# Optimization experiments

Hardware: AMD Instinct MI355X
Metric: run time of the kernel (lower is better)

Reference implementation:

```python
import jax, jax.numpy as jnp
import numpy as np

HSIG_SCALE = 0.16666667  # matches MyHSigmoid's * 0.16666667

def setup_inputs() -> dict:
    key = jax.random.key(0)
    k = jax.random.split(key, 5)
    B, C, H, W, MID = 32, 256, 56, 56, 64
    return {
        "x": jax.random.normal(k[0], (B, C, H, W), dtype=jnp.float32),
        "w1": jax.random.normal(k[1], (MID, C), dtype=jnp.float32) * 0.05,
        "b1": jax.random.normal(k[2], (MID,), dtype=jnp.float32) * 0.05,
        "w2": jax.random.normal(k[3], (C, MID), dtype=jnp.float32) * 0.05,
        "b2": jax.random.normal(k[4], (C,), dtype=jnp.float32) * 0.05,
        "inject": 0, "current_epoch": 0, "counter": 0, "inject_index": 0,
    }

def reference(x, w1, b1, w2, b2, inject, current_epoch, counter, inject_index):
    # global average pool over H,W -> [B, C]
    pooled = jnp.mean(x, axis=(2, 3))
    # 1x1 conv reduce (GEMV) + ReLU
    h = jax.nn.relu(jnp.einsum('bc,mc->bm', pooled, w1) + b1)
    # 1x1 conv expand + hard-sigmoid (relu6(y+3) * 0.16666667)
    y = jnp.einsum('bm,cm->bc', h, w2) + b2
    gate = jnp.clip(y + 3.0, 0.0, 6.0) * HSIG_SCALE
    # broadcast channel gate over spatial dims
    return x * gate[:, :, None, None]
```

## Files before the change

### kernel.cpp

```cpp
#include <hip/hip_runtime.h>
#include <stdint.h>

#define BATCH 32
#define CH    256
#define MID   64
#define HW    3136
#define HWV   784

typedef __attribute__((ext_vector_type(4))) float fvec4;

__global__ __launch_bounds__(256) void se_pool(const fvec4* __restrict__ x,
                                               float* __restrict__ pooled) {
    const int p = blockIdx.x;
    const fvec4* base = x + (size_t)p * HWV;
    const int t = threadIdx.x;

    float sum = 0.0f;
    for (int i = t; i < HWV; i += 256) {
        fvec4 v = base[i];
        sum += v.x + v.y + v.z + v.w;
    }
    #pragma unroll
    for (int off = 32; off > 0; off >>= 1) sum += __shfl_down(sum, off, 64);

    __shared__ float part[4];
    if ((t & 63) == 0) part[t >> 6] = sum;
    __syncthreads();
    if (t == 0) {
        pooled[p] = (part[0] + part[1] + part[2] + part[3]) * (1.0f / (float)HW);
    }
}

__global__ __launch_bounds__(256) void se_gate_scale(
    const fvec4* __restrict__ x,
    const float* __restrict__ pooled,
    const float* __restrict__ w1, const float* __restrict__ b1,
    const float* __restrict__ w2, const float* __restrict__ b2,
    fvec4* __restrict__ out) {
    const int p = blockIdx.x;
    const int b = p >> 8;
    const int c = p & 255;
    const int t = threadIdx.x;
    const int m = t & 63;
    const int q = t >> 6;

    __shared__ float ps[CH];
    __shared__ float hp[4][MID];
    __shared__ float hs[MID];
    __shared__ float gsh;

    ps[t] = pooled[b * CH + t];
    __syncthreads();

    {
        float acc = 0.0f;
        const fvec4* wrow = (const fvec4*)(w1 + m * CH + q * 64);
        const float* pq = ps + q * 64;
        #pragma unroll
        for (int i = 0; i < 16; ++i) {
            fvec4 wv = wrow[i];
            acc += pq[4 * i + 0] * wv.x + pq[4 * i + 1] * wv.y +
                   pq[4 * i + 2] * wv.z + pq[4 * i + 3] * wv.w;
        }
        hp[q][m] = acc;
    }
    __syncthreads();
    if (t < MID) {
        hs[t] = fmaxf(b1[t] + hp[0][t] + hp[1][t] + hp[2][t] + hp[3][t], 0.0f);
    }
    __syncthreads();
    if (t < 64) {
        float v = hs[t] * w2[c * MID + t];
        #pragma unroll
        for (int off = 32; off > 0; off >>= 1) v += __shfl_down(v, off, 64);
        if (t == 0) {
            gsh = fminf(fmaxf(v + b2[c] + 3.0f, 0.0f), 6.0f) * 0.16666667f;
        }
    }
    __syncthreads();
    const float g = gsh;

    const fvec4* xb = x + (size_t)p * HWV;
    fvec4* ob = out + (size_t)p * HWV;
    for (int i = t; i < HWV; i += 256) {
        fvec4 v = xb[i];
        fvec4 r = { v.x * g, v.y * g, v.z * g, v.w * g };
        __builtin_nontemporal_store(r, ob + i);
    }
}

extern "C" void kernel_launch(void* const* d_in, const int* in_sizes, int n_in,
                              void* d_out, int out_size, void* d_ws, size_t ws_size,
                              hipStream_t stream) {
    (void)in_sizes; (void)n_in; (void)out_size; (void)ws_size;

    const float* x  = (const float*)d_in[0];
    const float* w1 = (const float*)d_in[1];
    const float* b1 = (const float*)d_in[2];
    const float* w2 = (const float*)d_in[3];
    const float* b2 = (const float*)d_in[4];

    float* pooled = (float*)d_ws;

    se_pool<<<BATCH * CH, 256, 0, stream>>>((const fvec4*)x, pooled);
    se_gate_scale<<<BATCH * CH, 256, 0, stream>>>((const fvec4*)x, pooled,
                                                  w1, b1, w2, b2, (fvec4*)d_out);
}
```

Measured before the change: 247.0 us.

## Fold first GEMV into pooling via atomics and prefetch x before gate compute

The pooling kernel now multiplies each pooled channel value by its w1 column and atomically accumulates into a per-batch hidden pre-activation buffer (zeroed with a memset). The first GEMV is no longer recomputed in every one of the 8192 scale blocks. The scale kernel issues its loads of x into registers before the gate computation, so memory latency overlaps the small GEMV and sync, and its loop is fully unrolled. The cost is 64 atomics per block with contention on 2048 addresses, plus an extra memset launch, and float atomics make the summation order nondeterministic.

```diff
diff --git a/kernel.cpp b/kernel.cpp
--- a/kernel.cpp
+++ b/kernel.cpp
@@ -9,12 +9,15 @@
 
 typedef __attribute__((ext_vector_type(4))) float fvec4;
 
-__global__ __launch_bounds__(256) void se_pool(const fvec4* __restrict__ x,
-                                               float* __restrict__ pooled) {
+__global__ __launch_bounds__(256) void se_pool_h(const fvec4* __restrict__ x,
+                                                 const float* __restrict__ w1,
+                                                 float* __restrict__ hpre) {
     const int p = blockIdx.x;
-    const fvec4* base = x + (size_t)p * HWV;
+    const int b = p >> 8;
+    const int c = p & 255;
     const int t = threadIdx.x;
 
+    const fvec4* base = x + (size_t)p * HWV;
     float sum = 0.0f;
     for (int i = t; i < HWV; i += 256) {
         fvec4 v = base[i];
@@ -26,67 +29,50 @@
     __shared__ float part[4];
     if ((t & 63) == 0) part[t >> 6] = sum;
     __syncthreads();
-    if (t == 0) {
-        pooled[p] = (part[0] + part[1] + part[2] + part[3]) * (1.0f / (float)HW);
+
+    if (t < MID) {
+        const float pv =
+            (part[0] + part[1] + part[2] + part[3]) * (1.0f / (float)HW);
+        atomicAdd(&hpre[b * MID + t], pv * w1[t * CH + c]);
     }
 }
 
-__global__ __launch_bounds__(256) void se_gate_scale(
-    const fvec4* __restrict__ x,
-    const float* __restrict__ pooled,
-    const float* __restrict__ w1, const float* __restrict__ b1,
-    const float* __restrict__ w2, const float* __restrict__ b2,
-    fvec4* __restrict__ out) {
+__global__ __launch_bounds__(256) void se_scale(const fvec4* __restrict__ x,
+                                                const float* __restrict__ hpre,
+                                                const float* __restrict__ b1,
+                                                const float* __restrict__ w2,
+                                                const float* __restrict__ b2,
+                                                fvec4* __restrict__ out) {
     const int p = blockIdx.x;
     const int b = p >> 8;
     const int c = p & 255;
     const int t = threadIdx.x;
-    const int m = t & 63;
-    const int q = t >> 6;
 
-    __shared__ float ps[CH];
-    __shared__ float hp[4][MID];
-    __shared__ float hs[MID];
+    const fvec4* xb = x + (size_t)p * HWV;
+    fvec4 v0 = xb[t];
+    fvec4 v1 = xb[t + 256];
+    fvec4 v2 = xb[t + 512];
+    fvec4 v3 = {0.f, 0.f, 0.f, 0.f};
+    if (t < 16) v3 = xb[t + 768];
+
     __shared__ float gsh;
-
-    ps[t] = pooled[b * CH + t];
-    __syncthreads();
-
-    {
-        float acc = 0.0f;
-        const fvec4* wrow = (const fvec4*)(w1 + m * CH + q * 64);
-        const float* pq = ps + q * 64;
+    if (t < MID) {
+        float hv = fmaxf(hpre[b * MID + t] + b1[t], 0.0f);
+        float yv = hv * w2[c * MID + t];
         #pragma unroll
-        for (int i = 0; i < 16; ++i) {
-            fvec4 wv = wrow[i];
-            acc += pq[4 * i + 0] * wv.x + pq[4 * i + 1] * wv.y +
-                   pq[4 * i + 2] * wv.z + pq[4 * i + 3] * wv.w;
-        }
-        hp[q][m] = acc;
-    }
-    __syncthreads();
-    if (t < MID) {
-        hs[t] = fmaxf(b1[t] + hp[0][t] + hp[1][t] + hp[2][t] + hp[3][t], 0.0f);
-    }
-    __syncthreads();
-    if (t < 64) {
-        float v = hs[t] * w2[c * MID + t];
-        #pragma unroll
-        for (int off = 32; off > 0; off >>= 1) v += __shfl_down(v, off, 64);
+        for (int off = 32; off > 0; off >>= 1) yv += __shfl_down(yv, off, 64);
         if (t == 0) {
-            gsh = fminf(fmaxf(v + b2[c] + 3.0f, 0.0f), 6.0f) * 0.16666667f;
+            gsh = fminf(fmaxf(yv + b2[c] + 3.0f, 0.0f), 6.0f) * 0.16666667f;
         }
     }
     __syncthreads();
     const float g = gsh;
 
-    const fvec4* xb = x + (size_t)p * HWV;
     fvec4* ob = out + (size_t)p * HWV;
-    for (int i = t; i < HWV; i += 256) {
-        fvec4 v = xb[i];
-        fvec4 r = { v.x * g, v.y * g, v.z * g, v.w * g };
-        __builtin_nontemporal_store(r, ob + i);
-    }
+    __builtin_nontemporal_store(v0 * g, ob + t);
+    __builtin_nontemporal_store(v1 * g, ob + t + 256);
+    __builtin_nontemporal_store(v2 * g, ob + t + 512);
+    if (t < 16) __builtin_nontemporal_store(v3 * g, ob + t + 768);
 }
 
 extern "C" void kernel_launch(void* const* d_in, const int* in_sizes, int n_in,
@@ -100,9 +86,10 @@
     const float* w2 = (const float*)d_in[3];
     const float* b2 = (const float*)d_in[4];
 
-    float* pooled = (float*)d_ws;
+    float* hpre = (float*)d_ws;
 
-    se_pool<<<BATCH * CH, 256, 0, stream>>>((const fvec4*)x, pooled);
-    se_gate_scale<<<BATCH * CH, 256, 0, stream>>>((const fvec4*)x, pooled,
-                                                  w1, b1, w2, b2, (fvec4*)d_out);
+    hipMemsetAsync(hpre, 0, BATCH * MID * sizeof(float), stream);
+    se_pool_h<<<BATCH * CH, 256, 0, stream>>>((const fvec4*)x, w1, hpre);
+    se_scale<<<BATCH * CH, 256, 0, stream>>>((const fvec4*)x, hpre,
+                                             b1, w2, b2, (fvec4*)d_out);
 }
```

New measurement: 211.4 us. -14.4%, faster.
